# Optimization experiments

Hardware: AMD Instinct MI355X
Metric: run time of the kernel (lower is better)

The kernel has to match this reference:

```python
import jax, jax.numpy as jnp
import numpy as np

B, S, E, H = 2, 2048, 1024, 16
D = E // H  # head_dim = 64


def setup_inputs() -> dict:
    key = jax.random.key(0)
    k1, k2, k3 = jax.random.split(key, 3)
    scale = 0.02
    return {
        "x": jax.random.normal(k1, (B, S, E), dtype=jnp.float32),
        "w_attn": jax.random.normal(k2, (E, 3 * E), dtype=jnp.float32) * scale,
        "b_attn": jnp.zeros((3 * E,), dtype=jnp.float32),
        "w_proj": jax.random.normal(k3, (E, E), dtype=jnp.float32) * scale,
        "b_proj": jnp.zeros((E,), dtype=jnp.float32),
    }


def reference(x, w_attn, b_attn, w_proj, b_proj):
    b, s, e = x.shape
    # fused QKV projection (HF Conv1D: x @ W + b)
    qkv = jnp.matmul(x, w_attn) + b_attn                      # [b, s, 3e]
    q, k, v = jnp.split(qkv, 3, axis=-1)

    def split_heads(t):
        return t.reshape(b, s, H, D).transpose(0, 2, 1, 3)    # [b, h, s, d]

    q, k, v = split_heads(q), split_heads(k), split_heads(v)

    # causal scaled dot-product attention (past_kv=None -> is_causal=True)
    scores = jnp.einsum("bhqd,bhkd->bhqk", q, k) / jnp.sqrt(jnp.float32(D))
    causal = jnp.tril(jnp.ones((s, s), dtype=bool))           # [s, s]
    scores = jnp.where(causal[None, None, :, :], scores, jnp.finfo(scores.dtype).min)
    probs = jax.nn.softmax(scores, axis=-1)
    ctx = jnp.einsum("bhqk,bhkd->bhqd", probs, v)             # [b, h, s, d]

    merged = ctx.transpose(0, 2, 1, 3).reshape(b, s, e)       # merge heads
    out = jnp.matmul(merged, w_proj) + b_proj                 # output proj
    return out
```

## Files before the change

kernel.cpp:

```cpp
#include <hip/hip_runtime.h>
#include <hip/hip_bf16.h>
#include <stdint.h>

#define B_ 2
#define S_ 2048
#define E_ 1024
#define H_ 16
#define D_ 64
#define M_ (B_*S_)
#define N3 (3*E_)

typedef unsigned short u16;
typedef float f32x4 __attribute__((ext_vector_type(4)));
typedef float f32x16 __attribute__((ext_vector_type(16)));
typedef __bf16 bf16x8 __attribute__((ext_vector_type(8)));
typedef u16 u16x8 __attribute__((ext_vector_type(8)));
typedef u16 u16x4 __attribute__((ext_vector_type(4)));
typedef uint32_t u32x4 __attribute__((ext_vector_type(4)));
typedef uint32_t u32x2 __attribute__((ext_vector_type(2)));

__device__ __forceinline__ u16 f2bf(float f){
    uint32_t u = __float_as_uint(f);
    u += 0x7fffu + ((u >> 16) & 1u);
    return (u16)(u >> 16);
}
__device__ __forceinline__ float bf2f(u16 v){ return __uint_as_float((uint32_t)v << 16); }

__device__ __forceinline__ void plswap(uint32_t& x, uint32_t& y){
#if __has_builtin(__builtin_amdgcn_permlane32_swap)
    u32x2 r = __builtin_amdgcn_permlane32_swap(x, y, false, false);
    x = r[0]; y = r[1];
#else
    uint32_t sx = (uint32_t)__shfl_xor((int)x, 32);
    uint32_t sy = (uint32_t)__shfl_xor((int)y, 32);
    bool hi = (threadIdx.x & 32) != 0;
    uint32_t nx = hi ? sy : x;
    uint32_t ny = hi ? y  : sx;
    x = nx; y = ny;
#endif
}

__global__ __launch_bounds__(256) void cast_f32_bf16(const float* __restrict__ in,
                                                     u16* __restrict__ out, int n4){
    int i = blockIdx.x * 256 + threadIdx.x;
    if (i < n4){
        float4 v = ((const float4*)in)[i];
        uint2 p;
        p.x = (uint32_t)f2bf(v.x) | ((uint32_t)f2bf(v.y) << 16);
        p.y = (uint32_t)f2bf(v.z) | ((uint32_t)f2bf(v.w) << 16);
        ((uint2*)out)[i] = p;
    }
}

__global__ __launch_bounds__(256) void transpose_cast2(const float* __restrict__ wa,
                                                       u16* __restrict__ oa,
                                                       const float* __restrict__ wp,
                                                       u16* __restrict__ op){
    __shared__ float t[32][33];
    int bid = blockIdx.x;
    const int NA = (N3/32)*(E_/32);
    const float* in; u16* out; int C; int bx, by;
    if (bid < NA){ in = wa; out = oa; C = N3; bx = bid % (N3/32); by = bid / (N3/32); }
    else { int k = bid - NA; in = wp; out = op; C = E_; bx = k % (E_/32); by = k / (E_/32); }
    int R = E_;
    int tx = threadIdx.x & 31, ty = threadIdx.x >> 5;
    int x = bx * 32 + tx;
    #pragma unroll
    for (int i = 0; i < 4; i++)
        t[ty + 8*i][tx] = in[(size_t)(by*32 + ty + 8*i) * C + x];
    __syncthreads();
    #pragma unroll
    for (int i = 0; i < 4; i++)
        out[(size_t)(bx*32 + ty + 8*i) * R + by*32 + tx] = f2bf(t[tx][ty + 8*i]);
}

template<bool OUT_BF16, bool QSCALE>
__global__ __launch_bounds__(256) void gemm_bf16(const u16* __restrict__ A,
                                                 const u16* __restrict__ BT,
                                                 const float* __restrict__ bias,
                                                 void* __restrict__ Cout,
                                                 int M, int N, int K){
    __shared__ u16 Al[128 * 64];
    __shared__ u16 Bl[128 * 64];
    int nb = N >> 7;
    int bm = blockIdx.x / nb, bn = blockIdx.x % nb;
    int row0 = bm << 7, col0 = bn << 7;
    int tid  = threadIdx.x;
    int wave = tid >> 6, lane = tid & 63;
    int wm = wave >> 1, wn = wave & 1;
    int lr = lane & 15;
    int g  = lane >> 4;
    int trow = tid >> 3;
    int chg  = ((tid & 7) ^ (trow & 7)) << 3;

    f32x4 acc[4][4] = {};

    for (int k0 = 0; k0 < K; k0 += 64){
        #pragma unroll
        for (int i = 0; i < 4; i++){
            const u16* ga = A + (size_t)(row0 + i*32 + trow) * K + k0 + chg;
            __builtin_amdgcn_global_load_lds(
                (const __attribute__((address_space(1))) void*)ga,
                (__attribute__((address_space(3))) void*)&Al[i*2048 + wave*512],
                16, 0, 0);
        }
        #pragma unroll
        for (int i = 0; i < 4; i++){
            const u16* gb = BT + (size_t)(col0 + i*32 + trow) * K + k0 + chg;
            __builtin_amdgcn_global_load_lds(
                (const __attribute__((address_space(1))) void*)gb,
                (__attribute__((address_space(3))) void*)&Bl[i*2048 + wave*512],
                16, 0, 0);
        }
        __syncthreads();

        #pragma unroll
        for (int ks = 0; ks < 2; ks++){
            bf16x8 af[4], bfr[4];
            #pragma unroll
            for (int m = 0; m < 4; m++){
                int row = wm*64 + m*16 + lr;
                af[m] = *(const bf16x8*)((const char*)Al + row*128 + (((ks*4 + g) ^ (row & 7)) << 4));
            }
            #pragma unroll
            for (int n = 0; n < 4; n++){
                int row = wn*64 + n*16 + lr;
                bfr[n] = *(const bf16x8*)((const char*)Bl + row*128 + (((ks*4 + g) ^ (row & 7)) << 4));
            }
            #pragma unroll
            for (int m = 0; m < 4; m++)
                #pragma unroll
                for (int n = 0; n < 4; n++)
                    acc[m][n] = __builtin_amdgcn_mfma_f32_16x16x32_bf16(af[m], bfr[n], acc[m][n], 0, 0, 0);
        }
        __syncthreads();
    }

    #pragma unroll
    for (int m = 0; m < 4; m++){
        int gr = row0 + wm*64 + m*16 + ((lane >> 4) << 2);
        #pragma unroll
        for (int n = 0; n < 4; n++){
            int gc = col0 + wn*64 + n*16 + lr;
            float bv = bias[gc];
            float sc = (QSCALE && gc < E_) ? 0.18033688011112042f : 1.0f;
            #pragma unroll
            for (int j = 0; j < 4; j++){
                float v = (acc[m][n][j] + bv) * sc;
                if (OUT_BF16) ((u16*)Cout)[(size_t)(gr + j) * N + gc] = f2bf(v);
                else          ((float*)Cout)[(size_t)(gr + j) * N + gc] = v;
            }
        }
    }
}

__global__ __launch_bounds__(512, 2) void attn_mfma8(const u16* __restrict__ qkv,
                                                     u16* __restrict__ ctx){
    __shared__ char smem[73728];
    u16* Kb = (u16*)smem;
    char* Vb = smem + 32768;
    float* Of = (float*)smem;
    float* Ll = (float*)(smem + 50688);

    int t = blockIdx.x;
    int p = t >> 5;
    int h = t & 15;
    int b = (t >> 4) & 1;

    int tid   = threadIdx.x;
    int wave  = tid >> 6, lane = tid & 63;
    int split = wave >> 1, wq = wave & 1;
    int l31   = lane & 31, hi = lane >> 5;
    int stp   = tid & 127;
    int kp    = stp >> 3, ch = stp & 7;

    const u16* base = qkv + (size_t)b * S_ * N3;
    const float MASKV = -30000.f;
    const float FMAX  = 14.f;

    #pragma unroll 1
    for (int half = 0; half < 2; ++half){
        int qb  = half ? (31 - p) : p;
        int q0  = qb << 6;
        int T   = 2*qb + 2;
        int nit = (2*qb + 5) >> 2;
        int qmin = q0 + wq*32;
        int qg   = qmin + l31;
        int diag = qmin >> 5;

        bf16x8 qf[4];
        #pragma unroll
        for (int s = 0; s < 4; s++)
            qf[s] = __builtin_bit_cast(bf16x8,
                *(const u16x8*)(base + (size_t)qg * N3 + h*64 + 16*s + 8*hi));

        f32x16 oacc[2] = {};
        float lrow = 0.f;
        u16x8 va, vb;

        if (split < T){
            int k0 = split << 5;
            #pragma unroll
            for (int c = 0; c < 2; c++){
                int row = c*16 + wq*8 + (lane >> 3);
                int chg = (lane & 7) ^ (row & 7);
                const u16* g = base + (size_t)(k0 + row) * N3 + E_ + h*64 + chg*8;
                __builtin_amdgcn_global_load_lds(
                    (const __attribute__((address_space(1))) void*)g,
                    (__attribute__((address_space(3))) void*)&Kb[split*4096 + c*1024 + wq*512], 16, 0, 0);
            }
            va = *(const u16x8*)(base + (size_t)(k0 + 2*kp)   * N3 + 2*E_ + h*64 + ch*8);
            vb = *(const u16x8*)(base + (size_t)(k0 + 2*kp+1) * N3 + 2*E_ + h*64 + ch*8);
            char* Vt = Vb + split*10240;
            #pragma unroll
            for (int e = 0; e < 8; e++){
                int d = ch*8 + e;
                int cp = ((kp >> 2) + (ch & 3)) & 3;
                uint32_t pkv = (uint32_t)va[e] | ((uint32_t)vb[e] << 16);
                *(uint32_t*)(Vt + d*80 + (cp << 4) + (kp & 3)*4) = pkv;
            }
        }
        __syncthreads();

        for (int it = 0; it < nit; ++it){
            int cur = it & 1, nxt = cur ^ 1;
            int kt  = it*4 + split;
            int ktn = kt + 4;
            bool pre = (ktn < T);

            if (pre){
                int kn0 = ktn << 5;
                #pragma unroll
                for (int c = 0; c < 2; c++){
                    int row = c*16 + wq*8 + (lane >> 3);
                    int chg = (lane & 7) ^ (row & 7);
                    const u16* g = base + (size_t)(kn0 + row) * N3 + E_ + h*64 + chg*8;
                    __builtin_amdgcn_global_load_lds(
                        (const __attribute__((address_space(1))) void*)g,
                        (__attribute__((address_space(3))) void*)&Kb[split*4096 + nxt*2048 + c*1024 + wq*512], 16, 0, 0);
                }
                va = *(const u16x8*)(base + (size_t)(kn0 + 2*kp)   * N3 + 2*E_ + h*64 + ch*8);
                vb = *(const u16x8*)(base + (size_t)(kn0 + 2*kp+1) * N3 + 2*E_ + h*64 + ch*8);
            }

            if (kt <= diag){
                int k0 = kt << 5;
                const char* Kl = (const char*)&Kb[split*4096 + cur*2048];
                const char* Vt = Vb + split*10240 + cur*5120;
                f32x16 sac = {};
                __builtin_amdgcn_s_setprio(1);
                #pragma unroll
                for (int s = 0; s < 4; s++){
                    bf16x8 kf = *(const bf16x8*)(Kl + l31*128 + (((2*s + hi) ^ (l31 & 7)) << 4));
                    sac = __builtin_amdgcn_mfma_f32_32x32x16_bf16(kf, qf[s], sac, 0, 0, 0);
                }
                __builtin_amdgcn_s_setprio(0);
                if (k0 + 31 > qmin){
                    #pragma unroll
                    for (int r = 0; r < 16; r++){
                        int kg = k0 + (r&3) + 8*(r>>2) + 4*hi;
                        if (kg > qg) sac[r] = MASKV;
                    }
                }
                float pv[16];
                #pragma unroll
                for (int r = 0; r < 16; r++) pv[r] = exp2f(sac[r] - FMAX);
                float ss[8];
                #pragma unroll
                for (int i = 0; i < 8; i++) ss[i] = pv[i] + pv[i+8];
                #pragma unroll
                for (int s2 = 4; s2 >= 1; s2 >>= 1)
                    #pragma unroll
                    for (int i = 0; i < s2; i++) ss[i] += ss[i+s2];
                lrow += ss[0];
                uint32_t pk[8];
                #pragma unroll
                for (int i = 0; i < 8; i++){
                    uint32_t r;
                    asm("v_cvt_pk_bf16_f32 %0, %1, %2" : "=v"(r) : "v"(pv[2*i]), "v"(pv[2*i+1]));
                    pk[i] = r;
                }
                bf16x8 pa[2];
                #pragma unroll
                for (int s = 0; s < 2; s++){
                    uint32_t a0 = pk[4*s+0], a1 = pk[4*s+2];
                    uint32_t b0 = pk[4*s+1], b1 = pk[4*s+3];
                    plswap(a0, a1);
                    plswap(b0, b1);
                    u32x4 pw; pw[0] = a0; pw[1] = b0; pw[2] = a1; pw[3] = b1;
                    pa[s] = __builtin_bit_cast(bf16x8, pw);
                }
                __builtin_amdgcn_s_setprio(1);
                #pragma unroll
                for (int dt = 0; dt < 2; dt++){
                    int d = dt*32 + l31;
                    #pragma unroll
                    for (int s = 0; s < 2; s++){
                        int c = ((2*s + hi) + ((d >> 3) & 3)) & 3;
                        bf16x8 vf = *(const bf16x8*)(Vt + d*80 + (c << 4));
                        oacc[dt] = __builtin_amdgcn_mfma_f32_32x32x16_bf16(vf, pa[s], oacc[dt], 0, 0, 0);
                    }
                }
                __builtin_amdgcn_s_setprio(0);
            }

            if (pre){
                char* Vt = Vb + split*10240 + nxt*5120;
                #pragma unroll
                for (int e = 0; e < 8; e++){
                    int d = ch*8 + e;
                    int cp = ((kp >> 2) + (ch & 3)) & 3;
                    uint32_t pkv = (uint32_t)va[e] | ((uint32_t)vb[e] << 16);
                    *(uint32_t*)(Vt + d*80 + (cp << 4) + (kp & 3)*4) = pkv;
                }
            }
            __syncthreads();
        }

        if (split != 0){
            float lsum = lrow + __shfl_xor(lrow, 32);
            int qi = wq*32 + l31;
            #pragma unroll
            for (int dt = 0; dt < 2; dt++)
                #pragma unroll
                for (int r = 0; r < 16; r++){
                    int d = dt*32 + (r&3) + 8*(r>>2) + 4*hi;
                    Of[(split-1)*4224 + qi*66 + d] = oacc[dt][r];
                }
            if (hi == 0) Ll[(split-1)*64 + qi] = lsum;
        }
        __syncthreads();

        if (split == 0){
            int qi = wq*32 + l31;
            float l = lrow + __shfl_xor(lrow, 32)
                    + Ll[0*64 + qi] + Ll[1*64 + qi] + Ll[2*64 + qi];
            float inv = 1.0f / l;
            u16* dst = ctx + (size_t)(b*S_ + q0 + qi) * E_ + h*64;
            #pragma unroll
            for (int dt = 0; dt < 2; dt++)
                #pragma unroll
                for (int rr = 0; rr < 4; rr++){
                    u16x4 o4;
                    #pragma unroll
                    for (int j = 0; j < 4; j++){
                        int r = rr*4 + j;
                        int d = dt*32 + j + 8*rr + 4*hi;
                        float o = oacc[dt][r] + Of[0*4224 + qi*66 + d]
                                + Of[1*4224 + qi*66 + d] + Of[2*4224 + qi*66 + d];
                        o4[j] = f2bf(o * inv);
                    }
                    *(u16x4*)(dst + dt*32 + rr*8 + 4*hi) = o4;
                }
        }
        __syncthreads();
    }
}

extern "C" void kernel_launch(void* const* d_in, const int* in_sizes, int n_in,
                              void* d_out, int out_size, void* d_ws, size_t ws_size,
                              hipStream_t stream){
    const float* x      = (const float*)d_in[0];
    const float* w_attn = (const float*)d_in[1];
    const float* b_attn = (const float*)d_in[2];
    const float* w_proj = (const float*)d_in[3];
    const float* b_proj = (const float*)d_in[4];
    float* out = (float*)d_out;

    char* ws = (char*)d_ws;
    u16* xb   = (u16*)(ws);
    u16* waT  = (u16*)(ws + 8u*1024*1024);
    u16* wpT  = (u16*)(ws + 14u*1024*1024);
    u16* qkv  = (u16*)(ws + 16u*1024*1024);
    u16* ctxb = (u16*)(ws + 40u*1024*1024);

    cast_f32_bf16<<<(M_*E_/4 + 255)/256, 256, 0, stream>>>(x, xb, M_*E_/4);
    transpose_cast2<<<(N3/32)*(E_/32) + (E_/32)*(E_/32), 256, 0, stream>>>(w_attn, waT, w_proj, wpT);
    gemm_bf16<true, true><<<(M_/128)*(N3/128), 256, 0, stream>>>(xb, waT, b_attn, qkv, M_, N3, E_);
    attn_mfma8<<<B_*H_*16, 512, 0, stream>>>(qkv, ctxb);
    gemm_bf16<false, false><<<(M_/128)*(E_/128), 256, 0, stream>>>(ctxb, wpT, b_proj, out, M_, E_, E_);
}
```

Measured before the change: 122.0 us.

## Use 256x256-tile pipelined GEMM with direct-to-LDS loads for QKV projection

Adds a new QKV projection GEMM with 256x256 output tiles per 512-thread block. It stages A and B tiles straight from global memory into LDS with global_load_lds and double-buffers them, overlapping the prefetch of the next K-slice with MFMA work in four phases per iteration. The larger tile is meant to raise data reuse per LDS byte and hide load latency. In exchange it uses 128KB of LDS per block and launches only 192 blocks, which limits occupancy and may leave some CUs idle.

```diff
diff --git a/kernel.cpp b/kernel.cpp
--- a/kernel.cpp
+++ b/kernel.cpp
@@ -74,6 +74,125 @@
         out[(size_t)(bx*32 + ty + 8*i) * R + by*32 + tx] = f2bf(t[tx][ty + 8*i]);
 }
 
+__device__ __forceinline__ void stage_half(char* L, int slotOff, const u16* gbase,
+                                           int K, int tid, int srow, int chg){
+    #pragma unroll
+    for (int l = 0; l < 2; l++){
+        const u16* gp = gbase + (size_t)(l*64 + srow) * K + chg;
+        __builtin_amdgcn_global_load_lds(
+            (const __attribute__((address_space(1))) void*)gp,
+            (__attribute__((address_space(3))) void*)(L + slotOff + l*8192 + tid*16),
+            16, 0, 0);
+    }
+}
+
+template<bool QSCALE>
+__global__ __launch_bounds__(512, 2) void gemm256_bf16(const u16* __restrict__ A,
+                                                       const u16* __restrict__ BT,
+                                                       const float* __restrict__ bias,
+                                                       u16* __restrict__ Cout,
+                                                       int M, int N, int K){
+    __shared__ char L[131072];
+    int nb = N >> 8;
+    int bm = blockIdx.x / nb, bn = blockIdx.x % nb;
+    int row0 = bm << 8, col0 = bn << 8;
+    int tid = threadIdx.x;
+    int w = tid >> 6, lane = tid & 63;
+    int wm = w >> 2, wn = w & 3;
+    int lr = lane & 15, g = lane >> 4;
+    int bh = wn >> 1;
+    int srow = tid >> 3;
+    int chg = ((tid & 7) ^ (srow & 7)) << 3;
+    int nt = K >> 6;
+
+    f32x4 acc[8][4] = {};
+
+    stage_half(L, 0*16384, A  + (size_t)(row0      )*K,      K, tid, srow, chg);
+    stage_half(L, 1*16384, A  + (size_t)(row0 + 128)*K,      K, tid, srow, chg);
+    stage_half(L, 65536 + 0*16384, BT + (size_t)(col0      )*K,      K, tid, srow, chg);
+    stage_half(L, 65536 + 1*16384, BT + (size_t)(col0 + 128)*K,      K, tid, srow, chg);
+    stage_half(L, 65536 + 2*16384, BT + (size_t)(col0      )*K + 64, K, tid, srow, chg);
+    stage_half(L, 65536 + 3*16384, BT + (size_t)(col0 + 128)*K + 64, K, tid, srow, chg);
+    asm volatile("s_waitcnt vmcnt(4)" ::: "memory");
+    asm volatile("s_barrier" ::: "memory");
+
+#define GPHASE(q, STAGE_STMT)                                                       \
+    {                                                                               \
+        bf16x8 af[2][2];                                                            \
+        _Pragma("unroll")                                                           \
+        for (int mr = 0; mr < 2; mr++){                                             \
+            _Pragma("unroll")                                                       \
+            for (int ks = 0; ks < 2; ks++){                                         \
+                int r = (q)*32 + mr*16 + lr;                                        \
+                af[mr][ks] = *(const bf16x8*)(L + aBase + r*128 + (((ks*4+g) ^ (r&7))<<4)); \
+            }                                                                       \
+        }                                                                           \
+        STAGE_STMT;                                                                 \
+        asm volatile("s_barrier" ::: "memory");                                     \
+        asm volatile("s_waitcnt lgkmcnt(0)" ::: "memory");                          \
+        __builtin_amdgcn_s_setprio(1);                                              \
+        _Pragma("unroll")                                                           \
+        for (int mr = 0; mr < 2; mr++){                                             \
+            _Pragma("unroll")                                                       \
+            for (int nr = 0; nr < 4; nr++){                                         \
+                _Pragma("unroll")                                                   \
+                for (int ks = 0; ks < 2; ks++)                                      \
+                    acc[(q)*2+mr][nr] = __builtin_amdgcn_mfma_f32_16x16x32_bf16(    \
+                        af[mr][ks], bfr[nr][ks], acc[(q)*2+mr][nr], 0, 0, 0);       \
+            }                                                                       \
+        }                                                                           \
+        __builtin_amdgcn_s_setprio(0);                                              \
+    }
+
+    for (int t = 0; t < nt; ++t){
+        int par   = t & 1;
+        int aBase = (par*2 + wm) * 16384;
+        int bBase = 65536 + (par*2 + bh) * 16384;
+
+        bf16x8 bfr[4][2];
+        #pragma unroll
+        for (int nr = 0; nr < 4; nr++){
+            #pragma unroll
+            for (int ks = 0; ks < 2; ks++){
+                int r = (wn & 1)*64 + nr*16 + lr;
+                bfr[nr][ks] = *(const bf16x8*)(L + bBase + r*128 + (((ks*4+g) ^ (r&7))<<4));
+            }
+        }
+
+        GPHASE(0, { if (t+1 < nt) stage_half(L, (((t+1)&1)*2 + 0)*16384,
+                        A + (size_t)(row0      )*K + (t+1)*64, K, tid, srow, chg); });
+        asm volatile("s_barrier" ::: "memory");
+        GPHASE(1, { if (t+1 < nt) stage_half(L, (((t+1)&1)*2 + 1)*16384,
+                        A + (size_t)(row0 + 128)*K + (t+1)*64, K, tid, srow, chg); });
+        asm volatile("s_barrier" ::: "memory");
+        GPHASE(2, { if (t+2 < nt) stage_half(L, 65536 + (par*2 + 0)*16384,
+                        BT + (size_t)(col0      )*K + (t+2)*64, K, tid, srow, chg); });
+        asm volatile("s_barrier" ::: "memory");
+        GPHASE(3, { if (t+2 < nt) stage_half(L, 65536 + (par*2 + 1)*16384,
+                        BT + (size_t)(col0 + 128)*K + (t+2)*64, K, tid, srow, chg); });
+        if (t+2 < nt)      { asm volatile("s_waitcnt vmcnt(4)" ::: "memory"); }
+        else if (t+1 < nt) { asm volatile("s_waitcnt vmcnt(0)" ::: "memory"); }
+        asm volatile("s_barrier" ::: "memory");
+    }
+#undef GPHASE
+
+    #pragma unroll
+    for (int mi = 0; mi < 8; mi++){
+        int gr = row0 + wm*128 + mi*16 + g*4;
+        #pragma unroll
+        for (int nr = 0; nr < 4; nr++){
+            int gc = col0 + wn*64 + nr*16 + lr;
+            float bv = bias[gc];
+            float sc = (QSCALE && gc < E_) ? 0.18033688011112042f : 1.0f;
+            #pragma unroll
+            for (int j = 0; j < 4; j++){
+                float v = (acc[mi][nr][j] + bv) * sc;
+                Cout[(size_t)(gr + j) * N + gc] = f2bf(v);
+            }
+        }
+    }
+}
+
 template<bool OUT_BF16, bool QSCALE>
 __global__ __launch_bounds__(256) void gemm_bf16(const u16* __restrict__ A,
                                                  const u16* __restrict__ BT,
@@ -376,7 +495,7 @@
 
     cast_f32_bf16<<<(M_*E_/4 + 255)/256, 256, 0, stream>>>(x, xb, M_*E_/4);
     transpose_cast2<<<(N3/32)*(E_/32) + (E_/32)*(E_/32), 256, 0, stream>>>(w_attn, waT, w_proj, wpT);
-    gemm_bf16<true, true><<<(M_/128)*(N3/128), 256, 0, stream>>>(xb, waT, b_attn, qkv, M_, N3, E_);
+    gemm256_bf16<true><<<(M_/256)*(N3/256), 512, 0, stream>>>(xb, waT, b_attn, qkv, M_, N3, E_);
     attn_mfma8<<<B_*H_*16, 512, 0, stream>>>(qkv, ctxb);
     gemm_bf16<false, false><<<(M_/128)*(E_/128), 256, 0, stream>>>(ctxb, wpT, b_proj, out, M_, E_, E_);
 }
```

Measured after the change: 114.2 us. 6.4% less time.
